# Performance work log

Measured on AMD Instinct MI355X. Metric: run time of the kernel, lower is better.

The kernel has to match this reference:

```python
import jax, jax.numpy as jnp
import numpy as np

EPS = 1e-5

def _neighbor_idx(H, W):
    # flat index of the 3x3 clamped neighborhood for each pixel, [H*W, 9]
    r = np.arange(H)[:, None, None]  # [H,1,1]
    c = np.arange(W)[None, :, None]  # [1,W,1]
    dr = np.repeat(np.array([-1, 0, 1]), 3)[None, None, :]  # [1,1,9]
    dc = np.tile(np.array([-1, 0, 1]), 3)[None, None, :]
    ri = np.clip(r + dr, 0, H - 1)
    ci = np.clip(c + dc, 0, W - 1)
    return jnp.asarray((ri * W + ci).reshape(H * W, 9))

def setup_inputs() -> dict:
    key = jax.random.key(0)
    ks = jax.random.split(key, 7)
    B, C, H, W = 16, 256, 80, 80
    s = 1.0 / np.sqrt(C)
    return {
        "x": jax.random.normal(ks[0], (B, C, H, W), jnp.float32),
        "Wq": jax.random.normal(ks[1], (C, C), jnp.float32) * s,
        "bq": jax.random.normal(ks[2], (C,), jnp.float32) * s,
        "Wk": jax.random.normal(ks[3], (C, C), jnp.float32) * s,
        "bk": jax.random.normal(ks[4], (C,), jnp.float32) * s,
        "Wv": jax.random.normal(ks[5], (C, C), jnp.float32) * s,
        "bv": jax.random.normal(ks[6], (C,), jnp.float32) * s,
    }

def reference(x, Wq, bq, Wk, bk, Wv, bv):
    B, C, H, W = x.shape
    N = H * W
    xf = x.reshape(B, C, N)
    # 1x1 convs as channel GEMMs
    q = jnp.einsum('oc,bcn->bno', Wq, xf) + bq          # [B,N,C]
    k = jnp.einsum('oc,bcn->bon', Wk, xf) + bk[:, None]  # [B,C,N]
    v = jnp.einsum('oc,bcn->bon', Wv, xf) + bv[:, None]  # [B,C,N]
    idx = _neighbor_idx(H, W)                            # [N,9]
    k_n = k[:, :, idx]                                   # [B,C,N,9]
    v_n = v[:, :, idx]                                   # [B,C,N,9]
    # raw attention scores (NOT softmaxed before AV, matching the source)
    scores = jnp.einsum('bnc,bcnq->bnq', q, k_n)         # [B,N,9]
    new_v = jnp.einsum('bnq,bcnq->bcn', scores, v_n).reshape(B, C, H, W)
    out9 = scores.reshape(B, H, W, 9)
    center = out9[..., 4]
    others_mean = (out9.sum(-1) - center) / 8.0
    output = jnp.stack([center, others_mean], axis=-1)   # [B,H,W,2]
    # residual + layer_norm over [H,W] (no affine), per (B,C)
    xr = x + new_v
    mu = xr.mean(axis=(-2, -1), keepdims=True)
    var = ((xr - mu) ** 2).mean(axis=(-2, -1), keepdims=True)
    x_out = (xr - mu) * jax.lax.rsqrt(var + EPS)
    return (output, x_out)
```

## Files before the change

kernel.cpp:

```cpp
#include <hip/hip_runtime.h>
#include <hip/hip_bf16.h>

using f32x4  = __attribute__((ext_vector_type(4))) float;
using short8 = __attribute__((ext_vector_type(8))) short;
using bf16   = __hip_bfloat16;

constexpr int BATCH = 16;
constexpr int CH    = 256;
constexpr int HH    = 80;
constexpr int WW    = 80;
constexpr int NPIX  = HH * WW;

__device__ __forceinline__ float b2f(unsigned short u) {
    union { unsigned int i; float f; } x;
    x.i = ((unsigned int)u) << 16;
    return x.f;
}

typedef __attribute__((address_space(3))) void  lds_void;
typedef __attribute__((address_space(1))) const void glb_void;
__device__ __forceinline__ void glds16(const void* g, void* l) {
    __builtin_amdgcn_global_load_lds((glb_void*)(unsigned long long)g,
                                     (lds_void*)(unsigned int)(unsigned long long)l,
                                     16, 0, 0);
}

__global__ __launch_bounds__(256) void convert_w(
    const float* __restrict__ Wq, const float* __restrict__ Wk,
    const float* __restrict__ Wv, bf16* __restrict__ Wb)
{
    const int elem = blockIdx.x * 256 + threadIdx.x;
    const int mat  = blockIdx.y;
    const float* src = (mat == 0) ? Wq : (mat == 1) ? Wk : Wv;
    Wb[(size_t)mat * CH * CH + elem] = __float2bfloat16(src[elem]);
}

__global__ __launch_bounds__(256) void transpose_cast(
    const float* __restrict__ x, bf16* __restrict__ xt, int b0)
{
    __shared__ float t[64][65];
    const int b  = b0 + blockIdx.z;
    const int n0 = blockIdx.x * 64;
    const int c0 = blockIdx.y * 64;
    const float* xb = x + (size_t)b * CH * NPIX;
    const int tid = threadIdx.x;

    {
        const int nl  = tid & 63;
        const int cl0 = tid >> 6;
        #pragma unroll
        for (int i = 0; i < 16; ++i) {
            const int cl = cl0 + i * 4;
            t[cl][nl] = xb[(size_t)(c0 + cl) * NPIX + n0 + nl];
        }
    }
    __syncthreads();
    {
        bf16* xtb = xt + (size_t)blockIdx.z * NPIX * CH;
        const int cp  = (tid & 15) * 4;
        const int nl0 = tid >> 4;
        #pragma unroll
        for (int i = 0; i < 4; ++i) {
            const int nl = nl0 + i * 16;
            ushort4 pk;
            #pragma unroll
            for (int j = 0; j < 4; ++j) {
                const bf16 h = __float2bfloat16(t[cp + j][nl]);
                ((unsigned short*)&pk)[j] = *(const unsigned short*)&h;
            }
            *(ushort4*)(xtb + (size_t)(n0 + nl) * CH + c0 + cp) = pk;
        }
    }
}

__global__ __launch_bounds__(256, 2) void qkv_mfma(
    const bf16* __restrict__ xt, const bf16* __restrict__ Wb,
    const float* __restrict__ bq, const float* __restrict__ bk,
    const float* __restrict__ bv,
    bf16* __restrict__ qt, bf16* __restrict__ kt, bf16* __restrict__ vt)
{
    const int bl = blockIdx.z;
    const int n0 = blockIdx.x * 128;
    const int o0 = blockIdx.y * 128;
    const bf16* A = xt + (size_t)bl * NPIX * CH;

    __shared__ char As[128 * 512];
    __shared__ char Bs[2][128 * 64];

    const int tid = threadIdx.x;
    const int wv  = tid >> 6, ln = tid & 63;
    const int wr  = wv >> 1,  wc = wv & 1;
    const int lm  = ln & 15,  lk = ln >> 4;

    #pragma unroll
    for (int t = 0; t < 16; ++t) {
        const int idx = t * 256 + tid;
        const int row = idx >> 5, pos = idx & 31;
        const int chk = pos ^ (row & 7);
        glds16(A + (size_t)(n0 + row) * CH + chk * 8, &As[idx * 16]);
    }

    auto stageB = [&](int buf, const bf16* Wm, int k0) {
        #pragma unroll
        for (int it = 0; it < 2; ++it) {
            const int idx = it * 256 + tid;
            const int row = idx >> 2, pos = idx & 3;
            const int chk = pos ^ ((row >> 1) & 3);
            glds16(Wm + (size_t)(o0 + row) * CH + k0 + chk * 8, &Bs[buf][idx * 16]);
        }
    };

    stageB(0, Wb, 0);
    int buf = 0;

    bf16* const outs[3] = { qt + (size_t)bl * CH * NPIX,
                            kt + (size_t)bl * CH * NPIX,
                            vt + (size_t)bl * CH * NPIX };
    const float* const biases[3] = { bq, bk, bv };

    #pragma unroll
    for (int m = 0; m < 3; ++m) {
        f32x4 acc[4][4];
        #pragma unroll
        for (int i = 0; i < 4; ++i)
            #pragma unroll
            for (int j = 0; j < 4; ++j)
                #pragma unroll
                for (int r = 0; r < 4; ++r) acc[i][j][r] = 0.f;

        #pragma unroll
        for (int t = 0; t < 8; ++t) {
            __syncthreads();
            const int s = m * 8 + t;
            if (s < 23) {
                const int ns = s + 1;
                stageB(buf ^ 1, Wb + (size_t)(ns >> 3) * CH * CH, (ns & 7) * 32);
            }

            short8 afr[4], bfr[4];
            #pragma unroll
            for (int i = 0; i < 4; ++i) {
                const int row = wr * 64 + i * 16 + lm;
                const int chunk = (t * 4 + lk) ^ (row & 7);
                afr[i] = *(const short8*)&As[row * 512 + chunk * 16];
            }
            #pragma unroll
            for (int j = 0; j < 4; ++j) {
                const int row = wc * 64 + j * 16 + lm;
                const int chk = lk ^ ((row >> 1) & 3);
                bfr[j] = *(const short8*)&Bs[buf][row * 64 + chk * 16];
            }
            #pragma unroll
            for (int i = 0; i < 4; ++i)
                #pragma unroll
                for (int j = 0; j < 4; ++j)
                    acc[i][j] = __builtin_amdgcn_mfma_f32_16x16x32_bf16(
                        afr[i], bfr[j], acc[i][j], 0, 0, 0);
            buf ^= 1;
        }

        bf16* out = outs[m];
        const float* bias = biases[m];
        #pragma unroll
        for (int j = 0; j < 4; ++j) {
            const int o = o0 + wc * 64 + j * 16 + lm;
            const float bs = bias[o];
            #pragma unroll
            for (int i = 0; i < 4; ++i) {
                const int nb = n0 + wr * 64 + i * 16 + lk * 4;
                ushort4 pk;
                #pragma unroll
                for (int r = 0; r < 4; ++r) {
                    const bf16 h = __float2bfloat16(acc[i][j][r] + bs);
                    ((unsigned short*)&pk)[r] = *(const unsigned short*)&h;
                }
                *(ushort4*)(out + (size_t)o * NPIX + nb) = pk;
            }
        }
    }
}

__global__ __launch_bounds__(256) void scores_kernel(
    const bf16* __restrict__ qt, const bf16* __restrict__ kt,
    float* __restrict__ scores, float* __restrict__ out0, int b0)
{
    const int tid   = threadIdx.x;
    const int wave  = tid >> 6;
    const int lane  = tid & 63;
    const int ql    = lane & 3;
    const int chunk = lane >> 2;

    const int qi = blockIdx.x * 16 + wave * 4 + ql;
    const int bl = blockIdx.y;
    const int b  = b0 + bl;
    const int n0 = qi * 4;
    const int r  = qi / 20;
    const int p0 = n0 - r * WW;

    const unsigned short* qp = (const unsigned short*)(qt + (size_t)bl * NPIX * CH)
                               + (size_t)chunk * 16 * NPIX;
    const unsigned short* kp = (const unsigned short*)(kt + (size_t)bl * NPIX * CH)
                               + (size_t)chunk * 16 * NPIX;

    const int rbm = max(r - 1, 0) * WW;
    const int rb0 = r * WW;
    const int rbp = min(r + 1, HH - 1) * WW;
    const bool eL = (p0 == 0), eR = (p0 == 76);

    float acc[4][9];
    #pragma unroll
    for (int px = 0; px < 4; ++px)
        #pragma unroll
        for (int j = 0; j < 9; ++j) acc[px][j] = 0.f;

    #pragma unroll 4
    for (int c = 0; c < 16; ++c) {
        const size_t cb = (size_t)c * NPIX;
        const ushort4 qv = *(const ushort4*)(qp + cb + n0);
        const float qf0 = b2f(qv.x), qf1 = b2f(qv.y), qf2 = b2f(qv.z), qf3 = b2f(qv.w);

        #pragma unroll
        for (int dr = 0; dr < 3; ++dr) {
            const int rb = (dr == 0) ? rbm : (dr == 1) ? rb0 : rbp;
            const short8 kw = *(const short8*)(kp + cb + rb + p0 - 2);
            const float w3 = b2f((unsigned short)kw[1]);
            const float w4 = b2f((unsigned short)kw[2]);
            const float w5 = b2f((unsigned short)kw[3]);
            const float w6 = b2f((unsigned short)kw[4]);
            const float w7 = b2f((unsigned short)kw[5]);
            const float w8 = b2f((unsigned short)kw[6]);

            acc[0][dr*3+0] += qf0 * w3;
            acc[0][dr*3+1] += qf0 * w4;
            acc[0][dr*3+2] += qf0 * w5;
            acc[1][dr*3+0] += qf1 * w4;
            acc[1][dr*3+1] += qf1 * w5;
            acc[1][dr*3+2] += qf1 * w6;
            acc[2][dr*3+0] += qf2 * w5;
            acc[2][dr*3+1] += qf2 * w6;
            acc[2][dr*3+2] += qf2 * w7;
            acc[3][dr*3+0] += qf3 * w6;
            acc[3][dr*3+1] += qf3 * w7;
            acc[3][dr*3+2] += qf3 * w8;
            if (eL) acc[0][dr*3+0] += qf0 * (w4 - w3);
            if (eR) acc[3][dr*3+2] += qf3 * (w7 - w8);
        }
    }

    #pragma unroll
    for (int px = 0; px < 4; ++px)
        #pragma unroll
        for (int j = 0; j < 9; ++j) {
            float v = acc[px][j];
            v += __shfl_xor(v, 4,  64);
            v += __shfl_xor(v, 8,  64);
            v += __shfl_xor(v, 16, 64);
            v += __shfl_xor(v, 32, 64);
            acc[px][j] = v;
        }

    float* sp = scores + (size_t)bl * 9 * NPIX;
    if (chunk < 9) {
        float4 v = { acc[0][chunk], acc[1][chunk], acc[2][chunk], acc[3][chunk] };
        *(float4*)(sp + (size_t)chunk * NPIX + n0) = v;
    } else if (chunk == 9) {
        float ssum[4];
        #pragma unroll
        for (int px = 0; px < 4; ++px) {
            float s = 0.f;
            #pragma unroll
            for (int j = 0; j < 9; ++j) s += acc[px][j];
            ssum[px] = s;
        }
        float* op = out0 + ((size_t)b * NPIX + n0) * 2;
        float4 o0v = { acc[0][4], (ssum[0] - acc[0][4]) * 0.125f,
                       acc[1][4], (ssum[1] - acc[1][4]) * 0.125f };
        float4 o1v = { acc[2][4], (ssum[2] - acc[2][4]) * 0.125f,
                       acc[3][4], (ssum[3] - acc[3][4]) * 0.125f };
        *(float4*)(op)     = o0v;
        *(float4*)(op + 4) = o1v;
    }
}

__global__ __launch_bounds__(320) void newv_ln(
    const float* __restrict__ x, const bf16* __restrict__ vt,
    const float* __restrict__ scores, float* __restrict__ xout, int b0)
{
    __shared__ __align__(16) unsigned short lds_v[2][NPIX];
    __shared__ float rsum[5][2], rsq[5][2];

    const int cp2 = blockIdx.x;
    const int bl  = blockIdx.y;
    const int b   = b0 + bl;
    const int tid = threadIdx.x;

    const int4* vsrc = (const int4*)(vt + ((size_t)bl * CH + cp2 * 2) * NPIX);
    const float* xrow0 = x + ((size_t)b * CH + cp2 * 2) * NPIX;
    const float* xrow1 = xrow0 + NPIX;
    const float* sb    = scores + (size_t)bl * 9 * NPIX;

    float4 xv0[5], xv1[5];
    #pragma unroll
    for (int i = 0; i < 5; ++i) {
        const int n0 = (tid + i * 320) * 4;
        xv0[i] = *(const float4*)(xrow0 + n0);
        xv1[i] = *(const float4*)(xrow1 + n0);
    }

    #pragma unroll
    for (int i = 0; i < 5; ++i)
        ((int4*)lds_v)[tid + i * 320] = vsrc[tid + i * 320];
    __syncthreads();

    float val0[20], val1[20];
    float sum0 = 0.f, sq0 = 0.f, sum1 = 0.f, sq1 = 0.f;
    #pragma unroll
    for (int it = 0; it < 5; ++it) {
        const int p   = tid + it * 320;
        const int n0  = p * 4;
        const int r   = p / 20;
        const int c0  = (p % 20) * 4;

        const int rm = max(r - 1, 0) * WW;
        const int r0 = r * WW;
        const int rp = min(r + 1, HH - 1) * WW;

        float4 s[9];
        #pragma unroll
        for (int j = 0; j < 9; ++j)
            s[j] = *(const float4*)(sb + (size_t)j * NPIX + n0);

        const int cA = max(c0 - 1, 0);
        const int cF = min(c0 + 4, WW - 1);

        #pragma unroll
        for (int pl = 0; pl < 2; ++pl) {
            const unsigned short* lv = lds_v[pl];
            float vm[6], v0[6], vp[6];
            {
                const ushort4 a = *(const ushort4*)&lv[rm + c0];
                vm[1] = b2f(a.x); vm[2] = b2f(a.y); vm[3] = b2f(a.z); vm[4] = b2f(a.w);
                vm[0] = b2f(lv[rm + cA]); vm[5] = b2f(lv[rm + cF]);
            }
            {
                const ushort4 a = *(const ushort4*)&lv[r0 + c0];
                v0[1] = b2f(a.x); v0[2] = b2f(a.y); v0[3] = b2f(a.z); v0[4] = b2f(a.w);
                v0[0] = b2f(lv[r0 + cA]); v0[5] = b2f(lv[r0 + cF]);
            }
            {
                const ushort4 a = *(const ushort4*)&lv[rp + c0];
                vp[1] = b2f(a.x); vp[2] = b2f(a.y); vp[3] = b2f(a.z); vp[4] = b2f(a.w);
                vp[0] = b2f(lv[rp + cA]); vp[5] = b2f(lv[rp + cF]);
            }

            const float4 xin = pl ? xv1[it] : xv0[it];
            #pragma unroll
            for (int px = 0; px < 4; ++px) {
                float a;
                a  = ((const float*)&s[0])[px] * vm[px]
                   + ((const float*)&s[1])[px] * vm[px + 1]
                   + ((const float*)&s[2])[px] * vm[px + 2];
                a += ((const float*)&s[3])[px] * v0[px]
                   + ((const float*)&s[4])[px] * v0[px + 1]
                   + ((const float*)&s[5])[px] * v0[px + 2];
                a += ((const float*)&s[6])[px] * vp[px]
                   + ((const float*)&s[7])[px] * vp[px + 1]
                   + ((const float*)&s[8])[px] * vp[px + 2];
                const float vv = ((const float*)&xin)[px] + a;
                if (pl == 0) { val0[it * 4 + px] = vv; sum0 += vv; sq0 += vv * vv; }
                else         { val1[it * 4 + px] = vv; sum1 += vv; sq1 += vv * vv; }
            }
        }
    }

    #pragma unroll
    for (int off = 32; off >= 1; off >>= 1) {
        sum0 += __shfl_xor(sum0, off, 64);
        sq0  += __shfl_xor(sq0,  off, 64);
        sum1 += __shfl_xor(sum1, off, 64);
        sq1  += __shfl_xor(sq1,  off, 64);
    }
    const int wave = tid >> 6, lane = tid & 63;
    if (lane == 0) {
        rsum[wave][0] = sum0; rsq[wave][0] = sq0;
        rsum[wave][1] = sum1; rsq[wave][1] = sq1;
    }
    __syncthreads();
    sum0 = rsum[0][0] + rsum[1][0] + rsum[2][0] + rsum[3][0] + rsum[4][0];
    sq0  = rsq[0][0]  + rsq[1][0]  + rsq[2][0]  + rsq[3][0]  + rsq[4][0];
    sum1 = rsum[0][1] + rsum[1][1] + rsum[2][1] + rsum[3][1] + rsum[4][1];
    sq1  = rsq[0][1]  + rsq[1][1]  + rsq[2][1]  + rsq[3][1]  + rsq[4][1];

    const float mu0   = sum0 * (1.f / NPIX);
    const float var0  = sq0 * (1.f / NPIX) - mu0 * mu0;
    const float rstd0 = rsqrtf(var0 + 1e-5f);
    const float mu1   = sum1 * (1.f / NPIX);
    const float var1  = sq1 * (1.f / NPIX) - mu1 * mu1;
    const float rstd1 = rsqrtf(var1 + 1e-5f);

    float* orow0 = xout + ((size_t)b * CH + cp2 * 2) * NPIX;
    float* orow1 = orow0 + NPIX;
    #pragma unroll
    for (int it = 0; it < 5; ++it) {
        const int n0 = (tid + it * 320) * 4;
        float4 o0, o1;
        #pragma unroll
        for (int px = 0; px < 4; ++px) {
            ((float*)&o0)[px] = (val0[it * 4 + px] - mu0) * rstd0;
            ((float*)&o1)[px] = (val1[it * 4 + px] - mu1) * rstd1;
        }
        *(float4*)(orow0 + n0) = o0;
        *(float4*)(orow1 + n0) = o1;
    }
}

extern "C" void kernel_launch(void* const* d_in, const int* in_sizes, int n_in,
                              void* d_out, int out_size, void* d_ws, size_t ws_size,
                              hipStream_t stream)
{
    const float* x  = (const float*)d_in[0];
    const float* Wq = (const float*)d_in[1];
    const float* bq = (const float*)d_in[2];
    const float* Wk = (const float*)d_in[3];
    const float* bk = (const float*)d_in[4];
    const float* Wv = (const float*)d_in[5];
    const float* bv = (const float*)d_in[6];

    float* out0 = (float*)d_out;
    float* xout = out0 + (size_t)BATCH * NPIX * 2;

    char* ws = (char*)d_ws;
    bf16* Wb = (bf16*)ws;
    ws += (size_t)3 * CH * CH * sizeof(bf16);

    const size_t fBF = (size_t)NPIX * CH * sizeof(bf16);
    const size_t fSC = (size_t)NPIX * 9 * sizeof(float);
    const size_t perBatch = 4 * fBF + fSC;

    size_t avail = ws_size - ((size_t)3 * CH * CH * sizeof(bf16));
    int NB = (int)(avail / perBatch);
    if (NB < 1)  NB = 1;
    if (NB > BATCH) NB = BATCH;

    bf16*  xt  = (bf16*)ws;
    bf16*  qtb = (bf16*)(ws + (size_t)NB * fBF);
    bf16*  ktb = (bf16*)(ws + (size_t)NB * fBF * 2);
    bf16*  vtb = (bf16*)(ws + (size_t)NB * fBF * 3);
    float* sc  = (float*)(ws + (size_t)NB * fBF * 4);

    convert_w<<<dim3(CH * CH / 256, 3), 256, 0, stream>>>(Wq, Wk, Wv, Wb);

    for (int b0 = 0; b0 < BATCH; b0 += NB) {
        const int cnb = (BATCH - b0 < NB) ? (BATCH - b0) : NB;

        transpose_cast<<<dim3(NPIX / 64, CH / 64, cnb), 256, 0, stream>>>(x, xt, b0);

        qkv_mfma<<<dim3(NPIX / 128, CH / 128, cnb), 256, 0, stream>>>(
            xt, Wb, bq, bk, bv, qtb, ktb, vtb);

        scores_kernel<<<dim3(100, cnb), 256, 0, stream>>>(qtb, ktb, sc, out0, b0);

        newv_ln<<<dim3(CH / 2, cnb), 320, 0, stream>>>(x, vtb, sc, xout, b0);
    }
}
```

Before: 272.8 us.

## Restructure QKV GEMM to K-chunked A staging with three concurrent accumulators

```diff
diff --git a/kernel.cpp b/kernel.cpp
--- a/kernel.cpp
+++ b/kernel.cpp
@@ -77,88 +77,100 @@
     const bf16* __restrict__ xt, const bf16* __restrict__ Wb,
     const float* __restrict__ bq, const float* __restrict__ bk,
     const float* __restrict__ bv,
-    bf16* __restrict__ qt, bf16* __restrict__ kt, bf16* __restrict__ vt)
+    bf16* __restrict__ qt, bf16* __restrict__ kt2, bf16* __restrict__ vt)
 {
     const int bl = blockIdx.z;
     const int n0 = blockIdx.x * 128;
     const int o0 = blockIdx.y * 128;
     const bf16* A = xt + (size_t)bl * NPIX * CH;
 
-    __shared__ char As[128 * 512];
-    __shared__ char Bs[2][128 * 64];
+    __shared__ char As[2][128 * 128];
+    __shared__ char Bs[2][128 * 128];
 
     const int tid = threadIdx.x;
     const int wv  = tid >> 6, ln = tid & 63;
     const int wr  = wv >> 1,  wc = wv & 1;
     const int lm  = ln & 15,  lk = ln >> 4;
 
-    #pragma unroll
-    for (int t = 0; t < 16; ++t) {
-        const int idx = t * 256 + tid;
-        const int row = idx >> 5, pos = idx & 31;
-        const int chk = pos ^ (row & 7);
-        glds16(A + (size_t)(n0 + row) * CH + chk * 8, &As[idx * 16]);
-    }
-
+    auto stageA = [&](int buf, int k0) {
+        #pragma unroll
+        for (int it = 0; it < 4; ++it) {
+            const int idx = it * 256 + tid;
+            const int row = idx >> 3, pos = idx & 7;
+            const int chk = pos ^ (row & 7);
+            glds16(A + (size_t)(n0 + row) * CH + k0 + chk * 8, &As[buf][idx * 16]);
+        }
+    };
     auto stageB = [&](int buf, const bf16* Wm, int k0) {
         #pragma unroll
-        for (int it = 0; it < 2; ++it) {
+        for (int it = 0; it < 4; ++it) {
             const int idx = it * 256 + tid;
-            const int row = idx >> 2, pos = idx & 3;
-            const int chk = pos ^ ((row >> 1) & 3);
+            const int row = idx >> 3, pos = idx & 7;
+            const int chk = pos ^ (row & 7);
             glds16(Wm + (size_t)(o0 + row) * CH + k0 + chk * 8, &Bs[buf][idx * 16]);
         }
     };
 
+    stageA(0, 0);
     stageB(0, Wb, 0);
-    int buf = 0;
-
-    bf16* const outs[3] = { qt + (size_t)bl * CH * NPIX,
-                            kt + (size_t)bl * CH * NPIX,
-                            vt + (size_t)bl * CH * NPIX };
-    const float* const biases[3] = { bq, bk, bv };
-
-    #pragma unroll
-    for (int m = 0; m < 3; ++m) {
-        f32x4 acc[4][4];
+    int ab = 0, bb = 0;
+
+    f32x4 acc[3][4][4];
+    #pragma unroll
+    for (int m = 0; m < 3; ++m)
         #pragma unroll
         for (int i = 0; i < 4; ++i)
             #pragma unroll
             for (int j = 0; j < 4; ++j)
                 #pragma unroll
-                for (int r = 0; r < 4; ++r) acc[i][j][r] = 0.f;
-
-        #pragma unroll
-        for (int t = 0; t < 8; ++t) {
+                for (int r = 0; r < 4; ++r) acc[m][i][j][r] = 0.f;
+
+    #pragma unroll
+    for (int ktl = 0; ktl < 4; ++ktl) {
+        #pragma unroll
+        for (int m = 0; m < 3; ++m) {
             __syncthreads();
-            const int s = m * 8 + t;
-            if (s < 23) {
-                const int ns = s + 1;
-                stageB(buf ^ 1, Wb + (size_t)(ns >> 3) * CH * CH, (ns & 7) * 32);
-            }
-
-            short8 afr[4], bfr[4];
-            #pragma unroll
-            for (int i = 0; i < 4; ++i) {
-                const int row = wr * 64 + i * 16 + lm;
-                const int chunk = (t * 4 + lk) ^ (row & 7);
-                afr[i] = *(const short8*)&As[row * 512 + chunk * 16];
-            }
-            #pragma unroll
-            for (int j = 0; j < 4; ++j) {
-                const int row = wc * 64 + j * 16 + lm;
-                const int chk = lk ^ ((row >> 1) & 3);
-                bfr[j] = *(const short8*)&Bs[buf][row * 64 + chk * 16];
-            }
-            #pragma unroll
-            for (int i = 0; i < 4; ++i)
+            const int s = ktl * 3 + m;
+            if (s < 11) {
+                const int sn = s + 1;
+                const int kn = sn / 3, mn = sn % 3;
+                stageB(bb ^ 1, Wb + (size_t)mn * CH * CH, kn * 64);
+                if (m == 2) stageA(ab ^ 1, kn * 64);
+            }
+
+            #pragma unroll
+            for (int kk = 0; kk < 2; ++kk) {
+                short8 afr[4], bfr[4];
                 #pragma unroll
-                for (int j = 0; j < 4; ++j)
-                    acc[i][j] = __builtin_amdgcn_mfma_f32_16x16x32_bf16(
-                        afr[i], bfr[j], acc[i][j], 0, 0, 0);
-            buf ^= 1;
-        }
-
+                for (int i = 0; i < 4; ++i) {
+                    const int row  = wr * 64 + i * 16 + lm;
+                    const int slot = (kk * 4 + lk) ^ (row & 7);
+                    afr[i] = *(const short8*)&As[ab][row * 128 + slot * 16];
+                }
+                #pragma unroll
+                for (int j = 0; j < 4; ++j) {
+                    const int row  = wc * 64 + j * 16 + lm;
+                    const int slot = (kk * 4 + lk) ^ (row & 7);
+                    bfr[j] = *(const short8*)&Bs[bb][row * 128 + slot * 16];
+                }
+                #pragma unroll
+                for (int i = 0; i < 4; ++i)
+                    #pragma unroll
+                    for (int j = 0; j < 4; ++j)
+                        acc[m][i][j] = __builtin_amdgcn_mfma_f32_16x16x32_bf16(
+                            afr[i], bfr[j], acc[m][i][j], 0, 0, 0);
+            }
+            bb ^= 1;
+            if (m == 2) ab ^= 1;
+        }
+    }
+
+    bf16* const outs[3] = { qt  + (size_t)bl * CH * NPIX,
+                            kt2 + (size_t)bl * CH * NPIX,
+                            vt  + (size_t)bl * CH * NPIX };
+    const float* const biases[3] = { bq, bk, bv };
+    #pragma unroll
+    for (int m = 0; m < 3; ++m) {
         bf16* out = outs[m];
         const float* bias = biases[m];
         #pragma unroll
@@ -171,7 +183,7 @@
                 ushort4 pk;
                 #pragma unroll
                 for (int r = 0; r < 4; ++r) {
-                    const bf16 h = __float2bfloat16(acc[i][j][r] + bs);
+                    const bf16 h = __float2bfloat16(acc[m][i][j][r] + bs);
                     ((unsigned short*)&pk)[r] = *(const unsigned short*)&h;
                 }
                 *(ushort4*)(out + (size_t)o * NPIX + nb) = pk;
```

After: 322.5 us. +18.2%, slower.
